# Kernel optimization log

Hardware: AMD Instinct MI355X
Metric: run time of the kernel (lower is better)

The kernel has to match this reference:

```python
import jax, jax.numpy as jnp
import numpy as np

DIM, N_HEAD, DK, DV = 1024, 16, 64, 64
B, S = 1, 4096


def setup_inputs() -> dict:
    key = jax.random.key(0)
    ks = jax.random.split(key, 9)
    sd = 0.02
    return {
        "x": jax.random.normal(ks[0], (B, S, DIM), dtype=jnp.float32),
        "Wq": jax.random.normal(ks[1], (DIM, N_HEAD * DK), dtype=jnp.float32) * sd,
        "bq": jnp.zeros((N_HEAD * DK,), dtype=jnp.float32),
        "Wk": jax.random.normal(ks[2], (DIM, N_HEAD * DK), dtype=jnp.float32) * sd,
        "bk": jnp.zeros((N_HEAD * DK,), dtype=jnp.float32),
        "Wv": jax.random.normal(ks[3], (DIM, N_HEAD * DV), dtype=jnp.float32) * sd,
        "bv": jnp.zeros((N_HEAD * DV,), dtype=jnp.float32),
        "Wo": jax.random.normal(ks[4], (N_HEAD * DV, DIM), dtype=jnp.float32) * sd,
        "bo": jnp.zeros((DIM,), dtype=jnp.float32),
    }


def reference(x, Wq, bq, Wk, bk, Wv, bv, Wo, bo):
    b, s, _ = x.shape
    scale = DK ** (-0.5)
    # projections -> [b, h, s, d]
    q = (x @ Wq + bq).reshape(b, s, N_HEAD, DK).transpose(0, 2, 1, 3)
    k = (x @ Wk + bk).reshape(b, s, N_HEAD, DK).transpose(0, 2, 1, 3)
    v = (x @ Wv + bv).reshape(b, s, N_HEAD, DV).transpose(0, 2, 1, 3)
    attn = jnp.einsum("bhqd,bhkd->bhqk", q, k) * scale  # [b,h,s,s]
    attn = jax.nn.softmax(attn, axis=-1)
    out = jnp.einsum("bhqk,bhkd->bhqd", attn, v)  # [b,h,s,dv]
    out = out.transpose(0, 2, 1, 3).reshape(b, s, N_HEAD * DV)
    return out @ Wo + bo
```

## Files before the change

### kernel.cpp

```cpp
#include <hip/hip_runtime.h>
#include <hip/hip_bf16.h>
#include <hip/hip_fp16.h>

#define SEQ 4096
#define DIM 1024
#define NH 16
#define NT (SEQ / 64)

typedef __attribute__((ext_vector_type(4))) float f32x4;
typedef __attribute__((ext_vector_type(16))) float f32x16;
typedef __attribute__((ext_vector_type(8))) _Float16 half8;
typedef __attribute__((ext_vector_type(4))) _Float16 half4;

typedef const unsigned __attribute__((address_space(1)))* gas_t;
typedef unsigned __attribute__((address_space(3)))* las_t;

#if __has_builtin(__builtin_amdgcn_exp2f)
#define EXP2(x) __builtin_amdgcn_exp2f(x)
#else
#define EXP2(x) exp2f(x)
#endif

#define SMC 0.18033688f

__global__ __launch_bounds__(256) void prep_all(const float* __restrict__ x,
                                                _Float16* __restrict__ xh,
                                                const float* __restrict__ W0,
                                                const float* __restrict__ W1,
                                                const float* __restrict__ W2,
                                                const float* __restrict__ W3,
                                                _Float16* __restrict__ T0,
                                                _Float16* __restrict__ T1,
                                                _Float16* __restrict__ T2,
                                                _Float16* __restrict__ T3) {
  if (blockIdx.z == 4) {
    const int blkid = blockIdx.x * 32 + blockIdx.y;
#pragma unroll
    for (int u = 0; u < 4; u++) {
      int i = blkid * 4096 + u * 1024 + threadIdx.x * 4;
      float4 v = *reinterpret_cast<const float4*>(x + i);
      half4 h;
      h[0] = (_Float16)v.x; h[1] = (_Float16)v.y;
      h[2] = (_Float16)v.z; h[3] = (_Float16)v.w;
      *reinterpret_cast<half4*>(xh + i) = h;
    }
    return;
  }
  const float* W = blockIdx.z == 0 ? W0 : blockIdx.z == 1 ? W1 : blockIdx.z == 2 ? W2 : W3;
  _Float16* Wt = blockIdx.z == 0 ? T0 : blockIdx.z == 1 ? T1 : blockIdx.z == 2 ? T2 : T3;
  __shared__ float t[32][33];
  int bx = blockIdx.x * 32;
  int by = blockIdx.y * 32;
  int tx = threadIdx.x & 31, ty = threadIdx.x >> 5;
#pragma unroll
  for (int i = 0; i < 4; i++)
    t[ty + i * 8][tx] = W[(by + ty + i * 8) * DIM + bx + tx];
  __syncthreads();
#pragma unroll
  for (int i = 0; i < 4; i++)
    Wt[(bx + ty + i * 8) * DIM + by + tx] = (_Float16)t[tx][ty + i * 8];
}

template <int MODE>
__device__ __forceinline__ void gemm_body(const _Float16* __restrict__ A,
                                          const _Float16* __restrict__ Bt,
                                          const float* __restrict__ bias,
                                          void* __restrict__ outp,
                                          int M, int N, int Kd, int bmb, int bnb) {
  __shared__ __align__(16) _Float16 As[128][32];
  __shared__ __align__(16) _Float16 Bs[128][32];
  const int tid = threadIdx.x, lane = tid & 63, w = tid >> 6;
  const int bm = bmb * 128, bn = bnb * 128;
  const int l15 = lane & 15, g = lane >> 4, kb = g * 8;
  const int wr = (w >> 1) * 64, wc = (w & 1) * 64;
  const int lr = lane >> 2;
  const int lc = (lane & 3) * 8;
  f32x4 acc[4][4] = {};

  for (int k0 = 0; k0 < Kd; k0 += 32) {
    __syncthreads();
    const _Float16* as0 = A + (size_t)(bm + w * 32 + lr) * Kd + k0 + lc;
    __builtin_amdgcn_global_load_lds((gas_t)(const void*)as0,
                                     (las_t)(void*)&As[w * 32][0], 16, 0, 0);
    __builtin_amdgcn_global_load_lds((gas_t)(const void*)(as0 + (size_t)16 * Kd),
                                     (las_t)(void*)&As[w * 32 + 16][0], 16, 0, 0);
    const _Float16* bs0 = Bt + (size_t)(bn + w * 32 + lr) * Kd + k0 + lc;
    __builtin_amdgcn_global_load_lds((gas_t)(const void*)bs0,
                                     (las_t)(void*)&Bs[w * 32][0], 16, 0, 0);
    __builtin_amdgcn_global_load_lds((gas_t)(const void*)(bs0 + (size_t)16 * Kd),
                                     (las_t)(void*)&Bs[w * 32 + 16][0], 16, 0, 0);
    __syncthreads();

    half8 af[4], bf[4];
#pragma unroll
    for (int i = 0; i < 4; i++)
      af[i] = *reinterpret_cast<const half8*>(&As[wr + i * 16 + l15][kb]);
#pragma unroll
    for (int j = 0; j < 4; j++)
      bf[j] = *reinterpret_cast<const half8*>(&Bs[wc + j * 16 + l15][kb]);
    __builtin_amdgcn_s_setprio(1);
#pragma unroll
    for (int i = 0; i < 4; i++)
#pragma unroll
      for (int j = 0; j < 4; j++)
        acc[i][j] = __builtin_amdgcn_mfma_f32_16x16x32_f16(af[i], bf[j], acc[i][j], 0, 0, 0);
    __builtin_amdgcn_s_setprio(0);
  }

  const int gswap = ((g & 1) << 1) | (g >> 1);
#pragma unroll
  for (int i = 0; i < 4; i++)
#pragma unroll
    for (int j = 0; j < 4; j++) {
      const int col = bn + wc + j * 16 + l15;
      if (MODE == 2) {
        const int rowP = bm + wr + i * 16 + gswap * 4;
        half4 hv;
#pragma unroll
        for (int r = 0; r < 4; r++) hv[r] = (_Float16)(acc[i][j][r] + bias[col]);
        *reinterpret_cast<half4*>(&((_Float16*)outp)[(size_t)col * M + rowP]) = hv;
      } else {
        const int row0 = bm + wr + i * 16 + g * 4;
#pragma unroll
        for (int r = 0; r < 4; r++) {
          float vv = acc[i][j][r] + bias[col];
          if (MODE == 0) {
            _Float16* O = (_Float16*)outp;
            O[(((col >> 6) * SEQ) + row0 + r) * 64 + (col & 63)] = (_Float16)vv;
          } else {
            float* O = (float*)outp;
            O[(size_t)(row0 + r) * N + col] = vv;
          }
        }
      }
    }
}

__global__ __launch_bounds__(256) void gemm_qkv(const _Float16* __restrict__ A,
                                                const _Float16* __restrict__ WqT,
                                                const _Float16* __restrict__ WkT,
                                                const _Float16* __restrict__ WvT,
                                                const float* __restrict__ bq,
                                                const float* __restrict__ bk,
                                                const float* __restrict__ bv,
                                                _Float16* __restrict__ Qd,
                                                _Float16* __restrict__ Kd,
                                                _Float16* __restrict__ Vd) {
  if (blockIdx.z == 0)
    gemm_body<0>(A, WqT, bq, (void*)Qd, SEQ, DIM, DIM, blockIdx.x, blockIdx.y);
  else if (blockIdx.z == 1)
    gemm_body<0>(A, WkT, bk, (void*)Kd, SEQ, DIM, DIM, blockIdx.x, blockIdx.y);
  else
    gemm_body<2>(A, WvT, bv, (void*)Vd, SEQ, DIM, DIM, blockIdx.x, blockIdx.y);
}

__global__ __launch_bounds__(256) void gemm_out(const _Float16* __restrict__ A,
                                                const _Float16* __restrict__ Bt,
                                                const float* __restrict__ bias,
                                                float* __restrict__ out) {
  gemm_body<1>(A, Bt, bias, (void*)out, SEQ, DIM, DIM, blockIdx.x, blockIdx.y);
}

__global__ __launch_bounds__(512) void attn_fwd(const _Float16* __restrict__ Q,
                                                const _Float16* __restrict__ Kh,
                                                const _Float16* __restrict__ Vt_g,
                                                _Float16* __restrict__ Og) {
  __shared__ __align__(16) _Float16 Ks[3][64][72];
  __shared__ __align__(16) _Float16 Vs[3][64][72];
  const int hh = blockIdx.y;
  const int q0 = blockIdx.x * 256;
  const int tid = threadIdx.x, lane = tid & 63, w = tid >> 6;
  const int l31 = lane & 31, hq = lane >> 5, h8 = hq * 8;

  const int qrow = q0 + w * 32 + l31;
  const _Float16* qp = Q + ((size_t)hh * SEQ + qrow) * 64;
  half8 qf[4];
#pragma unroll
  for (int d = 0; d < 4; d++)
    qf[d] = *reinterpret_cast<const half8*>(qp + d * 16 + h8);

  f32x16 o[2] = {};
  float m = -1e30f, lsum = 0.f, negmC = 1e30f;
  const f32x16 kZero16 = {};

  const int srow = tid >> 3, sc8 = (tid & 7) * 8;
  const _Float16* kbase = Kh + (size_t)hh * SEQ * 64;
  const _Float16* vbase = Vt_g + (size_t)hh * 64 * SEQ;

  uint4 kr, vr;
  auto LOADKV = [&](int kt2) {
    kr = *reinterpret_cast<const uint4*>(kbase + (size_t)(kt2 * 64 + srow) * 64 + sc8);
    vr = *reinterpret_cast<const uint4*>(vbase + (size_t)srow * SEQ + kt2 * 64 + sc8);
  };
  auto STAGE = [&](int buf) {
    *reinterpret_cast<uint4*>(&Ks[buf][srow][sc8]) = kr;
    *reinterpret_cast<uint4*>(&Vs[buf][srow][sc8]) = vr;
  };

  auto QK = [&](int tile, f32x16 (&sf)[2]) {
    const int b = tile % 3;
    __builtin_amdgcn_s_setprio(1);
    {
      half8 kf0 = *reinterpret_cast<const half8*>(&Ks[b][l31][h8]);
      half8 kf1 = *reinterpret_cast<const half8*>(&Ks[b][32 + l31][h8]);
      sf[0] = __builtin_amdgcn_mfma_f32_32x32x16_f16(kf0, qf[0], kZero16, 0, 0, 0);
      sf[1] = __builtin_amdgcn_mfma_f32_32x32x16_f16(kf1, qf[0], kZero16, 0, 0, 0);
    }
#pragma unroll
    for (int d = 1; d < 4; d++) {
      half8 kf0 = *reinterpret_cast<const half8*>(&Ks[b][l31][d * 16 + h8]);
      half8 kf1 = *reinterpret_cast<const half8*>(&Ks[b][32 + l31][d * 16 + h8]);
      sf[0] = __builtin_amdgcn_mfma_f32_32x32x16_f16(kf0, qf[d], sf[0], 0, 0, 0);
      sf[1] = __builtin_amdgcn_mfma_f32_32x32x16_f16(kf1, qf[d], sf[1], 0, 0, 0);
    }
    __builtin_amdgcn_s_setprio(0);
  };

  auto ITER = [&](int t, f32x16 (&scur)[2], f32x16 (&snext)[2]) {
    if (t + 1 < NT) QK(t + 1, snext);

    float t0 = fmaxf(fmaxf(scur[0][0], scur[0][1]), scur[0][2]);
    float t1 = fmaxf(fmaxf(scur[0][3], scur[0][4]), scur[0][5]);
    float t2 = fmaxf(fmaxf(scur[0][6], scur[0][7]), scur[0][8]);
    float t3 = fmaxf(fmaxf(scur[0][9], scur[0][10]), scur[0][11]);
    float t4 = fmaxf(fmaxf(scur[0][12], scur[0][13]), scur[0][14]);
    float t5 = fmaxf(fmaxf(scur[0][15], scur[1][0]), scur[1][1]);
    float t6 = fmaxf(fmaxf(scur[1][2], scur[1][3]), scur[1][4]);
    float t7 = fmaxf(fmaxf(scur[1][5], scur[1][6]), scur[1][7]);
    float t8 = fmaxf(fmaxf(scur[1][8], scur[1][9]), scur[1][10]);
    float t9 = fmaxf(fmaxf(scur[1][11], scur[1][12]), scur[1][13]);
    float ta = fmaxf(scur[1][14], scur[1][15]);
    float u0 = fmaxf(fmaxf(t0, t1), t2);
    float u1 = fmaxf(fmaxf(t3, t4), t5);
    float u2 = fmaxf(fmaxf(t6, t7), t8);
    float u3 = fmaxf(t9, ta);
    float pm = fmaxf(fmaxf(fmaxf(u0, u1), u2), u3);

    if (__any(pm > m + 64.f)) {
      pm = fmaxf(pm, __shfl_xor(pm, 32, 64));
      float mn = fmaxf(m, pm);
      float al = EXP2((m - mn) * SMC);
      m = mn;
      negmC = -mn * SMC;
      lsum *= al;
      o[0] *= al;
      o[1] *= al;
    }
    f32x16 pf0, pf1;
#pragma unroll
    for (int r = 0; r < 16; r++) {
      float p = EXP2(fmaf(scur[0][r], SMC, negmC));
      pf0[r] = p;
      lsum += p;
    }
#pragma unroll
    for (int r = 0; r < 16; r++) {
      float p = EXP2(fmaf(scur[1][r], SMC, negmC));
      pf1[r] = p;
      lsum += p;
    }
    half8 pb[4];
#pragma unroll
    for (int s = 0; s < 4; s++) {
      const int base = (s & 1) * 8;
      unsigned d0, d1, d2, d3;
      if (s < 2) {
        d0 = __builtin_bit_cast(unsigned, __builtin_amdgcn_cvt_pkrtz(pf0[base + 0], pf0[base + 1]));
        d1 = __builtin_bit_cast(unsigned, __builtin_amdgcn_cvt_pkrtz(pf0[base + 2], pf0[base + 3]));
        d2 = __builtin_bit_cast(unsigned, __builtin_amdgcn_cvt_pkrtz(pf0[base + 4], pf0[base + 5]));
        d3 = __builtin_bit_cast(unsigned, __builtin_amdgcn_cvt_pkrtz(pf0[base + 6], pf0[base + 7]));
      } else {
        d0 = __builtin_bit_cast(unsigned, __builtin_amdgcn_cvt_pkrtz(pf1[base + 0], pf1[base + 1]));
        d1 = __builtin_bit_cast(unsigned, __builtin_amdgcn_cvt_pkrtz(pf1[base + 2], pf1[base + 3]));
        d2 = __builtin_bit_cast(unsigned, __builtin_amdgcn_cvt_pkrtz(pf1[base + 4], pf1[base + 5]));
        d3 = __builtin_bit_cast(unsigned, __builtin_amdgcn_cvt_pkrtz(pf1[base + 6], pf1[base + 7]));
      }
      uint4 uu = {d0, d1, d2, d3};
      pb[s] = __builtin_bit_cast(half8, uu);
    }

    const int bv = t % 3;
    __builtin_amdgcn_s_setprio(1);
#pragma unroll
    for (int s = 0; s < 4; s++) {
      half8 va0 = *reinterpret_cast<const half8*>(&Vs[bv][l31][s * 16 + h8]);
      half8 va1 = *reinterpret_cast<const half8*>(&Vs[bv][32 + l31][s * 16 + h8]);
      o[0] = __builtin_amdgcn_mfma_f32_32x32x16_f16(va0, pb[s], o[0], 0, 0, 0);
      o[1] = __builtin_amdgcn_mfma_f32_32x32x16_f16(va1, pb[s], o[1], 0, 0, 0);
    }
    __builtin_amdgcn_s_setprio(0);

    if (t + 2 < NT) STAGE((t + 2) % 3);
    if (t + 3 < NT) LOADKV(t + 3);
    __syncthreads();
  };

  LOADKV(0); STAGE(0);
  LOADKV(1); STAGE(1);
  LOADKV(2);
  __syncthreads();

  f32x16 sfA[2], sfB[2];
  QK(0, sfA);
  for (int t = 0; t < NT; t += 2) {
    ITER(t, sfA, sfB);
    ITER(t + 1, sfB, sfA);
  }

  float ls = lsum + __shfl_xor(lsum, 32, 64);
  float rinv = 1.f / ls;
#pragma unroll
  for (int tile = 0; tile < 2; tile++)
#pragma unroll
    for (int rg = 0; rg < 4; rg++) {
      half4 hv;
#pragma unroll
      for (int j = 0; j < 4; j++) hv[j] = (_Float16)(o[tile][rg * 4 + j] * rinv);
      const int dv = tile * 32 + rg * 8 + 4 * hq;
      *reinterpret_cast<half4*>(&Og[(size_t)qrow * DIM + hh * 64 + dv]) = hv;
    }
}


extern "C" void kernel_launch(void* const* d_in, const int* in_sizes, int n_in,
                              void* d_out, int out_size, void* d_ws, size_t ws_size,
                              hipStream_t stream) {
  const float* x  = (const float*)d_in[0];
  const float* Wq = (const float*)d_in[1];
  const float* bq = (const float*)d_in[2];
  const float* Wk = (const float*)d_in[3];
  const float* bk = (const float*)d_in[4];
  const float* Wv = (const float*)d_in[5];
  const float* bv = (const float*)d_in[6];
  const float* Wo = (const float*)d_in[7];
  const float* bo = (const float*)d_in[8];

  char* ws = (char*)d_ws;
  _Float16* xh  = (_Float16*)ws;
  _Float16* WqT = (_Float16*)(ws + (size_t)SEQ * DIM * 2);
  _Float16* WkT = WqT + DIM * DIM;
  _Float16* WvT = WkT + DIM * DIM;
  _Float16* WoT = WvT + DIM * DIM;
  _Float16* Qd  = WoT + DIM * DIM;
  _Float16* Kd  = Qd + (size_t)SEQ * DIM;
  _Float16* Vd  = Kd + (size_t)SEQ * DIM;
  _Float16* Od  = Vd + (size_t)SEQ * DIM;

  prep_all<<<dim3(32, 32, 5), 256, 0, stream>>>(x, xh, Wq, Wk, Wv, Wo,
                                                WqT, WkT, WvT, WoT);

  gemm_qkv<<<dim3(SEQ / 128, DIM / 128, 3), 256, 0, stream>>>(
      xh, WqT, WkT, WvT, bq, bk, bv, Qd, Kd, Vd);

  attn_fwd<<<dim3(SEQ / 256, NH), 512, 0, stream>>>(Qd, Kd, Vd, Od);

  gemm_out<<<dim3(SEQ / 128, DIM / 128), 256, 0, stream>>>(Od, WoT, bo, (float*)d_out);
}
```

Baseline: 163.7 us.

## Split attention over KV range into two partitions with separate merge kernel

The attention kernel now processes half of the key/value tiles per block, using a third grid dimension, which doubles the number of blocks. Each partition writes its normalized partial output plus its running max and sum. A new merge kernel combines the two partials with softmax rescaling into the head-interleaved output. This aims to raise occupancy and latency hiding across CUs, at the cost of extra global traffic for partials and an additional kernel launch.

```diff
diff --git a/kernel.cpp b/kernel.cpp
--- a/kernel.cpp
+++ b/kernel.cpp
@@ -6,6 +6,8 @@
 #define DIM 1024
 #define NH 16
 #define NT (SEQ / 64)
+#define NSPLIT 2
+#define TPP (NT / NSPLIT)
 
 typedef __attribute__((ext_vector_type(4))) float f32x4;
 typedef __attribute__((ext_vector_type(16))) float f32x16;
@@ -164,10 +166,12 @@
 __global__ __launch_bounds__(512) void attn_fwd(const _Float16* __restrict__ Q,
                                                 const _Float16* __restrict__ Kh,
                                                 const _Float16* __restrict__ Vt_g,
-                                                _Float16* __restrict__ Og) {
+                                                _Float16* __restrict__ Op,
+                                                float2* __restrict__ Ml) {
   __shared__ __align__(16) _Float16 Ks[3][64][72];
   __shared__ __align__(16) _Float16 Vs[3][64][72];
   const int hh = blockIdx.y;
+  const int part = blockIdx.z;
   const int q0 = blockIdx.x * 256;
   const int tid = threadIdx.x, lane = tid & 63, w = tid >> 6;
   const int l31 = lane & 31, hq = lane >> 5, h8 = hq * 8;
@@ -216,24 +220,26 @@
     __builtin_amdgcn_s_setprio(0);
   };
 
+  const int t0 = part * TPP, t1 = t0 + TPP;
+
   auto ITER = [&](int t, f32x16 (&scur)[2], f32x16 (&snext)[2]) {
-    if (t + 1 < NT) QK(t + 1, snext);
-
-    float t0 = fmaxf(fmaxf(scur[0][0], scur[0][1]), scur[0][2]);
-    float t1 = fmaxf(fmaxf(scur[0][3], scur[0][4]), scur[0][5]);
-    float t2 = fmaxf(fmaxf(scur[0][6], scur[0][7]), scur[0][8]);
-    float t3 = fmaxf(fmaxf(scur[0][9], scur[0][10]), scur[0][11]);
-    float t4 = fmaxf(fmaxf(scur[0][12], scur[0][13]), scur[0][14]);
-    float t5 = fmaxf(fmaxf(scur[0][15], scur[1][0]), scur[1][1]);
-    float t6 = fmaxf(fmaxf(scur[1][2], scur[1][3]), scur[1][4]);
-    float t7 = fmaxf(fmaxf(scur[1][5], scur[1][6]), scur[1][7]);
-    float t8 = fmaxf(fmaxf(scur[1][8], scur[1][9]), scur[1][10]);
-    float t9 = fmaxf(fmaxf(scur[1][11], scur[1][12]), scur[1][13]);
-    float ta = fmaxf(scur[1][14], scur[1][15]);
-    float u0 = fmaxf(fmaxf(t0, t1), t2);
-    float u1 = fmaxf(fmaxf(t3, t4), t5);
-    float u2 = fmaxf(fmaxf(t6, t7), t8);
-    float u3 = fmaxf(t9, ta);
+    if (t + 1 < t1) QK(t + 1, snext);
+
+    float t0v = fmaxf(fmaxf(scur[0][0], scur[0][1]), scur[0][2]);
+    float t1v = fmaxf(fmaxf(scur[0][3], scur[0][4]), scur[0][5]);
+    float t2v = fmaxf(fmaxf(scur[0][6], scur[0][7]), scur[0][8]);
+    float t3v = fmaxf(fmaxf(scur[0][9], scur[0][10]), scur[0][11]);
+    float t4v = fmaxf(fmaxf(scur[0][12], scur[0][13]), scur[0][14]);
+    float t5v = fmaxf(fmaxf(scur[0][15], scur[1][0]), scur[1][1]);
+    float t6v = fmaxf(fmaxf(scur[1][2], scur[1][3]), scur[1][4]);
+    float t7v = fmaxf(fmaxf(scur[1][5], scur[1][6]), scur[1][7]);
+    float t8v = fmaxf(fmaxf(scur[1][8], scur[1][9]), scur[1][10]);
+    float t9v = fmaxf(fmaxf(scur[1][11], scur[1][12]), scur[1][13]);
+    float tav = fmaxf(scur[1][14], scur[1][15]);
+    float u0 = fmaxf(fmaxf(t0v, t1v), t2v);
+    float u1 = fmaxf(fmaxf(t3v, t4v), t5v);
+    float u2 = fmaxf(fmaxf(t6v, t7v), t8v);
+    float u3 = fmaxf(t9v, tav);
     float pm = fmaxf(fmaxf(fmaxf(u0, u1), u2), u3);
 
     if (__any(pm > m + 64.f)) {
@@ -290,25 +296,26 @@
     }
     __builtin_amdgcn_s_setprio(0);
 
-    if (t + 2 < NT) STAGE((t + 2) % 3);
-    if (t + 3 < NT) LOADKV(t + 3);
+    if (t + 2 < t1) STAGE((t + 2) % 3);
+    if (t + 3 < t1) LOADKV(t + 3);
     __syncthreads();
   };
 
-  LOADKV(0); STAGE(0);
-  LOADKV(1); STAGE(1);
-  LOADKV(2);
+  LOADKV(t0); STAGE(t0 % 3);
+  LOADKV(t0 + 1); STAGE((t0 + 1) % 3);
+  LOADKV(t0 + 2);
   __syncthreads();
 
   f32x16 sfA[2], sfB[2];
-  QK(0, sfA);
-  for (int t = 0; t < NT; t += 2) {
+  QK(t0, sfA);
+  for (int t = t0; t < t1; t += 2) {
     ITER(t, sfA, sfB);
     ITER(t + 1, sfB, sfA);
   }
 
   float ls = lsum + __shfl_xor(lsum, 32, 64);
   float rinv = 1.f / ls;
+  const size_t prow = ((size_t)part * NH + hh) * SEQ + qrow;
 #pragma unroll
   for (int tile = 0; tile < 2; tile++)
 #pragma unroll
@@ -317,8 +324,32 @@
 #pragma unroll
       for (int j = 0; j < 4; j++) hv[j] = (_Float16)(o[tile][rg * 4 + j] * rinv);
       const int dv = tile * 32 + rg * 8 + 4 * hq;
-      *reinterpret_cast<half4*>(&Og[(size_t)qrow * DIM + hh * 64 + dv]) = hv;
-    }
+      *reinterpret_cast<half4*>(&Op[prow * 64 + dv]) = hv;
+    }
+  if (hq == 0) Ml[prow] = make_float2(m, ls);
+}
+
+__global__ __launch_bounds__(256) void attn_merge(const _Float16* __restrict__ Op,
+                                                  const float2* __restrict__ Ml,
+                                                  _Float16* __restrict__ Og) {
+  const int gid = blockIdx.x * 256 + threadIdx.x;
+  const int dv4 = (gid & 15) * 4;
+  const int row = gid >> 4;
+  const int h = row >> 12, s = row & (SEQ - 1);
+  float2 a = Ml[row];
+  float2 b = Ml[(size_t)NH * SEQ + row];
+  float mm = fmaxf(a.x, b.x);
+  float w1 = a.y * EXP2((a.x - mm) * SMC);
+  float w2 = b.y * EXP2((b.x - mm) * SMC);
+  float rinv = 1.f / (w1 + w2);
+  w1 *= rinv; w2 *= rinv;
+  half4 o1 = *reinterpret_cast<const half4*>(&Op[(size_t)row * 64 + dv4]);
+  half4 o2 = *reinterpret_cast<const half4*>(&Op[((size_t)NH * SEQ + row) * 64 + dv4]);
+  half4 hv;
+#pragma unroll
+  for (int j = 0; j < 4; j++)
+    hv[j] = (_Float16)(w1 * (float)o1[j] + w2 * (float)o2[j]);
+  *reinterpret_cast<half4*>(&Og[(size_t)s * DIM + h * 64 + dv4]) = hv;
 }
 
 
@@ -345,6 +376,8 @@
   _Float16* Kd  = Qd + (size_t)SEQ * DIM;
   _Float16* Vd  = Kd + (size_t)SEQ * DIM;
   _Float16* Od  = Vd + (size_t)SEQ * DIM;
+  _Float16* Opart = Od + (size_t)SEQ * DIM;
+  float2*   Mlp   = (float2*)(Opart + (size_t)NSPLIT * NH * SEQ * 64);
 
   prep_all<<<dim3(32, 32, 5), 256, 0, stream>>>(x, xh, Wq, Wk, Wv, Wo,
                                                 WqT, WkT, WvT, WoT);
@@ -352,7 +385,8 @@
   gemm_qkv<<<dim3(SEQ / 128, DIM / 128, 3), 256, 0, stream>>>(
       xh, WqT, WkT, WvT, bq, bk, bv, Qd, Kd, Vd);
 
-  attn_fwd<<<dim3(SEQ / 256, NH), 512, 0, stream>>>(Qd, Kd, Vd, Od);
+  attn_fwd<<<dim3(SEQ / 256, NH, NSPLIT), 512, 0, stream>>>(Qd, Kd, Vd, Opart, Mlp);
+  attn_merge<<<(NH * SEQ * 16) / 256, 256, 0, stream>>>(Opart, Mlp, Od);
 
   gemm_out<<<dim3(SEQ / 128, DIM / 128), 256, 0, stream>>>(Od, WoT, bo, (float*)d_out);
 }
```

Measured after the change: 176.2 us. 1.08x slower.
